# Kernel tuning notes

Measured on AMD Instinct MI355X. Metric: run time of the kernel, lower is better.

## Reference

```python
import jax, jax.numpy as jnp
import numpy as np

B, Q, D, H, P, F = 16, 300, 256, 8, 4, 2048
HG = WG = 100          # feature-map height/width (hw = 10000, perfect square)
HW = HG * WG
DH = D // H
EPS = 1e-5


def _ln(x, g, b):
    m = x.mean(-1, keepdims=True)
    v = jnp.var(x, axis=-1, keepdims=True)
    return (x - m) * jax.lax.rsqrt(v + EPS) * g + b


def setup_inputs() -> dict:
    key = jax.random.key(0)
    ks = jax.random.split(key, 24)
    rn = lambda k, shape, s=0.02: jax.random.normal(k, shape, jnp.float32) * s
    return {
        "tgt": jax.random.normal(ks[0], (B, Q, D), jnp.float32),
        "memory": jax.random.normal(ks[1], (B, HW, D), jnp.float32),
        "in_proj_w": rn(ks[2], (D, 3 * D)), "in_proj_b": rn(ks[3], (3 * D,)),
        "out_proj_w": rn(ks[4], (D, D)), "out_proj_b": rn(ks[5], (D,)),
        "norm1_g": jnp.ones((D,), jnp.float32), "norm1_b": jnp.zeros((D,), jnp.float32),
        "ref_w": rn(ks[6], (D, 2)), "ref_b": rn(ks[7], (2,)),
        "off_w": rn(ks[8], (D, H * P * 2)), "off_b": rn(ks[9], (H * P * 2,)),
        "attw_w": rn(ks[10], (D, H * P)), "attw_b": rn(ks[11], (H * P,)),
        "vproj_w": rn(ks[12], (D, D)), "vproj_b": rn(ks[13], (D,)),
        "oproj_w": rn(ks[14], (D, D)), "oproj_b": rn(ks[15], (D,)),
        "norm2_g": jnp.ones((D,), jnp.float32), "norm2_b": jnp.zeros((D,), jnp.float32),
        "lin1_w": rn(ks[16], (D, F)), "lin1_b": rn(ks[17], (F,)),
        "lin2_w": rn(ks[18], (F, D)), "lin2_b": rn(ks[19], (D,)),
        "norm3_g": jnp.ones((D,), jnp.float32), "norm3_b": jnp.zeros((D,), jnp.float32),
    }


def reference(tgt, memory, in_proj_w, in_proj_b, out_proj_w, out_proj_b,
              norm1_g, norm1_b, ref_w, ref_b, off_w, off_b, attw_w, attw_b,
              vproj_w, vproj_b, oproj_w, oproj_b, norm2_g, norm2_b,
              lin1_w, lin1_b, lin2_w, lin2_b, norm3_g, norm3_b):
    # ---- self-attention (nn.MultiheadAttention, eval mode: dropout = identity)
    qkv = tgt @ in_proj_w + in_proj_b                      # [B,Q,3D]
    q, k, v = jnp.split(qkv, 3, axis=-1)
    q = q.reshape(B, Q, H, DH)
    k = k.reshape(B, Q, H, DH)
    v = v.reshape(B, Q, H, DH)
    scores = jnp.einsum('bqhd,bkhd->bhqk', q, k) / jnp.sqrt(jnp.float32(DH))
    attn = jax.nn.softmax(scores, axis=-1)
    sa = jnp.einsum('bhqk,bkhd->bqhd', attn, v).reshape(B, Q, D) @ out_proj_w + out_proj_b
    x = _ln(tgt + sa, norm1_g, norm1_b)

    # ---- reference points
    ref = jax.nn.sigmoid(x @ ref_w + ref_b)                # [B,Q,2] in (0,1)

    # ---- deformable cross-attention
    offs = (x @ off_w + off_b).reshape(B, Q, H, P, 2)
    wts = jax.nn.softmax((x @ attw_w + attw_b).reshape(B, Q, H, P), axis=-1)
    vals = (memory @ vproj_w + vproj_b).reshape(B, HW, H, DH)
    loc = jnp.clip(ref[:, :, None, None, :] + offs, 0.0, 1.0)
    sx = loc[..., 0] * (WG - 1)
    sy = loc[..., 1] * (HG - 1)
    x0 = jnp.floor(sx)
    y0 = jnp.floor(sy)
    x0i = jnp.clip(x0.astype(jnp.int32), 0, WG - 1)
    y0i = jnp.clip(y0.astype(jnp.int32), 0, HG - 1)
    x1i = jnp.clip(x0i + 1, 0, WG - 1)
    y1i = jnp.clip(y0i + 1, 0, HG - 1)
    wx1 = sx - x0
    wx0 = 1.0 - wx1
    wy1 = sy - y0
    wy0 = 1.0 - wy1
    bi = jnp.arange(B)[:, None, None, None]
    hi = jnp.arange(H)[None, None, :, None]

    def gather(yi, xi):                                    # [B,Q,H,P,DH]
        return vals[bi, yi * WG + xi, hi]

    samp = (gather(y0i, x0i) * (wx0 * wy0)[..., None]
            + gather(y1i, x0i) * (wx0 * wy1)[..., None]
            + gather(y0i, x1i) * (wx1 * wy0)[..., None]
            + gather(y1i, x1i) * (wx1 * wy1)[..., None])
    ca = (samp * wts[..., None]).sum(axis=3).reshape(B, Q, D) @ oproj_w + oproj_b
    x = _ln(x + ca, norm2_g, norm2_b)

    # ---- FFN
    ff = jax.nn.relu(x @ lin1_w + lin1_b) @ lin2_w + lin2_b
    return _ln(x + ff, norm3_g, norm3_b)
```

## Files before the change

kernel.cpp:

```cpp
#include <hip/hip_runtime.h>

#define NB   16
#define NQ   300
#define ND   256
#define NH   8
#define NP   4
#define NF   2048
#define NHW  10000
#define NWG  100
#define NROW 4800

typedef __attribute__((ext_vector_type(8))) short bf16x8;
typedef __attribute__((ext_vector_type(4))) float f32x4;

__device__ __forceinline__ unsigned short f2bf(float f) {
    unsigned u = __builtin_bit_cast(unsigned, f);
    u = (u + 0x7fffu + ((u >> 16) & 1u)) >> 16;
    return (unsigned short)u;
}
__device__ __forceinline__ float bf2f(unsigned short h) {
    unsigned u = ((unsigned)h) << 16;
    return __builtin_bit_cast(float, u);
}

__device__ __forceinline__ bf16x8 cvt8(float4 lo, float4 hi) {
    unsigned r0, r1, r2, r3;
    asm("v_cvt_pk_bf16_f32 %0, %1, %2" : "=v"(r0) : "v"(lo.x), "v"(lo.y));
    asm("v_cvt_pk_bf16_f32 %0, %1, %2" : "=v"(r1) : "v"(lo.z), "v"(lo.w));
    asm("v_cvt_pk_bf16_f32 %0, %1, %2" : "=v"(r2) : "v"(hi.x), "v"(hi.y));
    asm("v_cvt_pk_bf16_f32 %0, %1, %2" : "=v"(r3) : "v"(hi.z), "v"(hi.w));
    uint4 u = {r0, r1, r2, r3};
    return __builtin_bit_cast(bf16x8, u);
}

__device__ __forceinline__ void gl_lds16(const unsigned short* g, unsigned short* l) {
    __builtin_amdgcn_global_load_lds(
        (__attribute__((address_space(1))) const void*)g,
        (__attribute__((address_space(3))) void*)l,
        16, 0, 0);
}
__device__ __forceinline__ void gl_lds16f(const float* g, float* l) {
    __builtin_amdgcn_global_load_lds(
        (__attribute__((address_space(1))) const void*)g,
        (__attribute__((address_space(3))) void*)l,
        16, 0, 0);
}

__global__ __launch_bounds__(256) void transpose_cast(
    const float* __restrict__ w_in,  const float* __restrict__ w_out,
    const float* __restrict__ w_vp,  const float* __restrict__ w_op,
    const float* __restrict__ w_l1,  const float* __restrict__ w_l2,
    unsigned short* __restrict__ o_in, unsigned short* __restrict__ o_out,
    unsigned short* __restrict__ o_vp, unsigned short* __restrict__ o_op,
    unsigned short* __restrict__ o_l1, unsigned short* __restrict__ o_l2)
{
    __shared__ float ts[64][65];
    int b = blockIdx.x;
    const float* src; unsigned short* dst; int K, N, ncx;
    if      (b < 48)  { src = w_in;  dst = o_in;  K = 256;  N = 768;  ncx = 12; }
    else if (b < 64)  { src = w_out; dst = o_out; K = 256;  N = 256;  ncx = 4;  b -= 48; }
    else if (b < 80)  { src = w_vp;  dst = o_vp;  K = 256;  N = 256;  ncx = 4;  b -= 64; }
    else if (b < 96)  { src = w_op;  dst = o_op;  K = 256;  N = 256;  ncx = 4;  b -= 80; }
    else if (b < 224) { src = w_l1;  dst = o_l1;  K = 256;  N = 2048; ncx = 32; b -= 96; }
    else              { src = w_l2;  dst = o_l2;  K = 2048; N = 256;  ncx = 4;  b -= 224; }
    const int n0 = (b % ncx) * 64, k0 = (b / ncx) * 64;
    const int t = threadIdx.x;
    const int r = t >> 4, c = t & 15;
    #pragma unroll
    for (int j = 0; j < 4; j++) {
        float4 v = *(const float4*)(src + (long)(k0 + j * 16 + r) * N + n0 + c * 4);
        ts[j * 16 + r][c * 4 + 0] = v.x;
        ts[j * 16 + r][c * 4 + 1] = v.y;
        ts[j * 16 + r][c * 4 + 2] = v.z;
        ts[j * 16 + r][c * 4 + 3] = v.w;
    }
    __syncthreads();
    #pragma unroll
    for (int j = 0; j < 4; j++) {
        unsigned short o[4];
        #pragma unroll
        for (int i = 0; i < 4; i++)
            o[i] = f2bf(ts[c * 4 + i][j * 16 + r]);
        *(uint2*)(dst + (long)(n0 + j * 16 + r) * K + k0 + c * 4) = *(uint2*)o;
    }
}

__global__ __launch_bounds__(256) void prep_head(
    const float* __restrict__ rw, const float* __restrict__ rb,
    const float* __restrict__ ow, const float* __restrict__ ob,
    const float* __restrict__ aw, const float* __restrict__ ab,
    unsigned short* __restrict__ o_hd, float* __restrict__ o_hb)
{
    int id = blockIdx.x * 256 + threadIdx.x;
    if (id < 32768) {
        int n = id >> 8, k = id & 255;
        float v;
        if (n < 2)       v = rw[k * 2 + n];
        else if (n < 66) v = ow[k * 64 + (n - 2)];
        else if (n < 98) v = aw[k * 32 + (n - 66)];
        else             v = 0.0f;
        o_hd[id] = f2bf(v);
        return;
    }
    id -= 32768;
    if (id < 128) {
        float v;
        if (id < 2)       v = rb[id];
        else if (id < 66) v = ob[id - 2];
        else if (id < 98) v = ab[id - 66];
        else              v = 0.0f;
        o_hb[id] = v;
    }
}

__global__ __launch_bounds__(512, 2) void gemm_vproj_bs(
    const float* __restrict__ A, const unsigned short* __restrict__ Bt,
    const float* __restrict__ bias, unsigned short* __restrict__ Cout)
{
    __shared__ __align__(16) unsigned short Bs[128 * 512];
    __shared__ __align__(16) float As[2][16 * 256];

    const int t    = threadIdx.x;
    const int wave = t >> 6, lane = t & 63;
    const int l16  = lane & 15, quad = lane >> 4;
    const long m0  = (long)blockIdx.x * 640;

    {
        const unsigned short* bp = Bt + (long)(wave * 32 + l16) * 256 + (quad << 3);
        unsigned short* bw = &Bs[wave << 13];
        #pragma unroll
        for (int kf = 0; kf < 8; kf++) {
            gl_lds16(bp + kf * 32,            bw + kf * 512);
            gl_lds16(bp + kf * 32 + 16 * 256, bw + 4096 + kf * 512);
        }
    }

    const float* aG = A + (m0 + l16) * 256 + wave * 32 + (quad << 3);
    auto issueA = [&](int it, int buf) {
        const float* g = aG + (long)it * 16 * 256;
        gl_lds16f(g,     &As[buf][wave * 512]);
        gl_lds16f(g + 4, &As[buf][wave * 512 + 256]);
    };

    issueA(0, 0);
    __syncthreads();

    float4 bj0 = *(const float4*)&bias[wave * 32 + (quad << 2)];
    float4 bj1 = *(const float4*)&bias[wave * 32 + 16 + (quad << 2)];

    const unsigned short* bF0 = &Bs[(wave << 13)] + (lane << 3);
    const unsigned short* bF1 = bF0 + 4096;

    for (int it = 0; it < 40; ++it) {
        const int cur = it & 1;
        if (it + 1 < 40) {
            issueA(it + 1, cur ^ 1);
            asm volatile("s_waitcnt vmcnt(2)" ::: "memory");
        } else {
            asm volatile("s_waitcnt vmcnt(0)" ::: "memory");
        }
        __builtin_amdgcn_sched_barrier(0);

        f32x4 acc0 = {0.f, 0.f, 0.f, 0.f}, acc1 = {0.f, 0.f, 0.f, 0.f};
        #pragma unroll
        for (int kf = 0; kf < 8; kf++) {
            const float4 alo = *(const float4*)&As[cur][kf * 512 + (lane << 2)];
            const float4 ahi = *(const float4*)&As[cur][kf * 512 + 256 + (lane << 2)];
            const bf16x8 af  = cvt8(alo, ahi);
            const bf16x8 bv0 = *(const bf16x8*)(bF0 + kf * 512);
            const bf16x8 bv1 = *(const bf16x8*)(bF1 + kf * 512);
            acc0 = __builtin_amdgcn_mfma_f32_16x16x32_bf16(bv0, af, acc0, 0, 0, 0);
            acc1 = __builtin_amdgcn_mfma_f32_16x16x32_bf16(bv1, af, acc1, 0, 0, 0);
        }

        const long gr = m0 + (long)it * 16 + l16;
        unsigned short* cp = Cout + gr * 256 + wave * 32 + (quad << 2);
        {
            unsigned short o[4] = {f2bf(acc0[0] + bj0.x), f2bf(acc0[1] + bj0.y),
                                   f2bf(acc0[2] + bj0.z), f2bf(acc0[3] + bj0.w)};
            *(uint2*)cp = *(uint2*)o;
        }
        {
            unsigned short o[4] = {f2bf(acc1[0] + bj1.x), f2bf(acc1[1] + bj1.y),
                                   f2bf(acc1[2] + bj1.z), f2bf(acc1[3] + bj1.w)};
            *(uint2*)(cp + 16) = *(uint2*)o;
        }

        __builtin_amdgcn_s_barrier();
    }
}

template <int RELU, int OUTBF, int SPLITK, int TM, int TN>
__global__ __launch_bounds__(TM * 4, 4) void gemm_bt(
    const float* __restrict__ A, const unsigned short* __restrict__ Bt,
    const float* __restrict__ bias, void* __restrict__ Cout,
    int M, int N, int K)
{
    constexpr int W   = TM / 16;
    constexpr int NFB = TN / 16;
    constexpr int WN  = TN / 64;
    constexpr int WM  = W / WN;
    constexpr int AI  = (TM / 16) / WM;
    constexpr int BPW = NFB / W;

    __shared__ __align__(16) unsigned short As[2][W * 512];
    __shared__ __align__(16) unsigned short Bs[2][NFB * 512];

    const int t    = threadIdx.x;
    const long m0  = (long)blockIdx.y * TM;
    const int  n0  = blockIdx.x * TN;
    const int  wave = t >> 6, lane = t & 63;
    const int  l16 = lane & 15, quad = lane >> 4;
    const int  wmi = wave / WN, wni = wave % WN;
    const int  wm  = wmi * (AI * 16);
    const int  wn  = wni * 64;
    const int  fA  = wmi * AI;
    const int  fB  = wni * 4;

    f32x4 acc[AI][4] = {};

    const int kChunk = K / SPLITK;
    const int kBeg   = (SPLITK > 1) ? blockIdx.z * kChunk : 0;
    const int nk     = kChunk / 32;

    const long aRow   = m0 + wave * 16 + l16;
    const bool aValid = (aRow < M);
    const float* aP   = A + aRow * (long)K + kBeg + (quad << 3);
    unsigned short* aW = &As[0][(wave << 9) + (lane << 3)];

    const unsigned short* bP =
        Bt + (long)(n0 + wave * (16 * BPW) + l16) * K + kBeg + (quad << 3);
    unsigned short* bW = &Bs[0][wave * BPW * 512];

    float4 la0 = make_float4(0.f, 0.f, 0.f, 0.f);
    float4 la1 = make_float4(0.f, 0.f, 0.f, 0.f);

    auto loadA = [&](int kt) {
        if (aValid) {
            la0 = *(const float4*)(aP + kt * 32);
            la1 = *(const float4*)(aP + kt * 32 + 4);
        }
    };
    auto writeA = [&](int buf) {
        const bf16x8 v = cvt8(la0, la1);
        *(bf16x8*)(aW + buf * (W * 512)) = v;
    };
    auto issueB = [&](int kt, int buf) {
        #pragma unroll
        for (int j = 0; j < BPW; j++)
            gl_lds16(bP + kt * 32 + (long)j * 16 * K,
                     bW + buf * (NFB * 512) + j * 512);
    };

    issueB(0, 0);
    loadA(0);
    writeA(0);
    __syncthreads();

    for (int kt = 0; kt < nk; kt++) {
        const int cur = kt & 1;
        if (kt + 1 < nk) {
            issueB(kt + 1, cur ^ 1);
            loadA(kt + 1);
        }

        bf16x8 af[AI], bfr[4];
        #pragma unroll
        for (int i = 0; i < AI; i++)
            af[i] = *(const bf16x8*)&As[cur][(fA + i) * 512 + (lane << 3)];
        #pragma unroll
        for (int j = 0; j < 4; j++)
            bfr[j] = *(const bf16x8*)&Bs[cur][(fB + j) * 512 + (lane << 3)];
        #pragma unroll
        for (int i = 0; i < AI; i++)
            #pragma unroll
            for (int j = 0; j < 4; j++)
                acc[i][j] = __builtin_amdgcn_mfma_f32_16x16x32_bf16(
                    bfr[j], af[i], acc[i][j], 0, 0, 0);

        if (kt + 1 < nk) {
            writeA(cur ^ 1);
            __syncthreads();
        }
    }

    float4 bj[4];
    #pragma unroll
    for (int j = 0; j < 4; j++)
        bj[j] = *(const float4*)&bias[n0 + wn + j * 16 + (quad << 2)];

    float* outp = (float*)Cout;
    float bscale = 1.0f;
    if (SPLITK > 1) {
        outp += (size_t)blockIdx.z * M * N;
        bscale = (blockIdx.z == 0) ? 1.0f : 0.0f;
    }

    #pragma unroll
    for (int i = 0; i < AI; i++) {
        const long gr = m0 + wm + i * 16 + l16;
        if (gr < M) {
            #pragma unroll
            for (int j = 0; j < 4; j++) {
                float4 v;
                v.x = acc[i][j][0] + bscale * bj[j].x;
                v.y = acc[i][j][1] + bscale * bj[j].y;
                v.z = acc[i][j][2] + bscale * bj[j].z;
                v.w = acc[i][j][3] + bscale * bj[j].w;
                if (RELU) {
                    v.x = fmaxf(v.x, 0.f); v.y = fmaxf(v.y, 0.f);
                    v.z = fmaxf(v.z, 0.f); v.w = fmaxf(v.w, 0.f);
                }
                const int gc = n0 + wn + j * 16 + (quad << 2);
                if (OUTBF) {
                    unsigned short o[4] = {f2bf(v.x), f2bf(v.y), f2bf(v.z), f2bf(v.w)};
                    *(uint2*)((unsigned short*)Cout + gr * N + gc) = *(uint2*)o;
                } else {
                    *(float4*)(outp + gr * N + gc) = v;
                }
            }
        }
    }
}

__global__ __launch_bounds__(256) void attn_kernel(
    const float* __restrict__ qkv, float* __restrict__ sa)
{
    __shared__ union {
        struct {
            unsigned short Ks[304][40];
            unsigned short Qs[64][40];
        } s;
        unsigned short Ps[4][16][328];
    } u;
    __shared__ unsigned short Vt[32][328];

    const int bh = blockIdx.y;
    const int b  = bh >> 3, h = bh & 7;
    const int q0 = blockIdx.x * 64;
    const int t  = threadIdx.x;

    for (int idx = t; idx < 304 * 8; idx += 256) {
        const int r = idx >> 3, c4 = (idx & 7) << 2;
        if (r < NQ) {
            const float4 kv = *(const float4*)(qkv + ((long)(b * NQ + r)) * 768 + 256 + h * 32 + c4);
            u.s.Ks[r][c4 + 0] = f2bf(kv.x); u.s.Ks[r][c4 + 1] = f2bf(kv.y);
            u.s.Ks[r][c4 + 2] = f2bf(kv.z); u.s.Ks[r][c4 + 3] = f2bf(kv.w);
        } else {
            u.s.Ks[r][c4 + 0] = 0; u.s.Ks[r][c4 + 1] = 0;
            u.s.Ks[r][c4 + 2] = 0; u.s.Ks[r][c4 + 3] = 0;
        }
    }
    for (int idx = t; idx < NQ * 8; idx += 256) {
        const int key = idx >> 3, dq = (idx & 7) << 2;
        const float4 vv = *(const float4*)(qkv + ((long)(b * NQ + key)) * 768 + 512 + h * 32 + dq);
        Vt[dq + 0][key] = f2bf(vv.x); Vt[dq + 1][key] = f2bf(vv.y);
        Vt[dq + 2][key] = f2bf(vv.z); Vt[dq + 3][key] = f2bf(vv.w);
    }
    for (int idx = t; idx < 32 * 20; idx += 256)
        Vt[idx / 20][300 + idx % 20] = 0;
    for (int idx = t; idx < 64 * 8; idx += 256) {
        const int r = idx >> 3, c4 = (idx & 7) << 2;
        const int q = q0 + r;
        if (q < NQ) {
            const float4 qv = *(const float4*)(qkv + ((long)(b * NQ + q)) * 768 + h * 32 + c4);
            u.s.Qs[r][c4 + 0] = f2bf(qv.x); u.s.Qs[r][c4 + 1] = f2bf(qv.y);
            u.s.Qs[r][c4 + 2] = f2bf(qv.z); u.s.Qs[r][c4 + 3] = f2bf(qv.w);
        } else {
            u.s.Qs[r][c4 + 0] = 0; u.s.Qs[r][c4 + 1] = 0;
            u.s.Qs[r][c4 + 2] = 0; u.s.Qs[r][c4 + 3] = 0;
        }
    }
    __syncthreads();

    const int wave = t >> 6, lane = t & 63;
    const int l16 = lane & 15, quad = lane >> 4;
    const float scale = 0.1767766952966369f;

    const bf16x8 aq = *(const bf16x8*)&u.s.Qs[wave * 16 + l16][quad * 8];
    f32x4 sacc[19];
    #pragma unroll
    for (int kt = 0; kt < 19; kt++) {
        const bf16x8 bk = *(const bf16x8*)&u.s.Ks[kt * 16 + l16][quad * 8];
        sacc[kt] = __builtin_amdgcn_mfma_f32_16x16x32_bf16(
            aq, bk, (f32x4){0.f, 0.f, 0.f, 0.f}, 0, 0, 0);
    }

    float inv[4];
    #pragma unroll
    for (int r = 0; r < 4; r++) {
        float m = -1e30f;
        #pragma unroll
        for (int kt = 0; kt < 19; kt++) {
            float s = sacc[kt][r] * scale;
            if (kt == 18 && l16 >= 12) s = -1e30f;
            sacc[kt][r] = s;
            m = fmaxf(m, s);
        }
        m = fmaxf(m, __shfl_xor(m, 1)); m = fmaxf(m, __shfl_xor(m, 2));
        m = fmaxf(m, __shfl_xor(m, 4)); m = fmaxf(m, __shfl_xor(m, 8));
        float sum = 0.f;
        #pragma unroll
        for (int kt = 0; kt < 19; kt++) {
            float p = __expf(sacc[kt][r] - m);
            sacc[kt][r] = p;
            sum += p;
        }
        sum += __shfl_xor(sum, 1); sum += __shfl_xor(sum, 2);
        sum += __shfl_xor(sum, 4); sum += __shfl_xor(sum, 8);
        inv[r] = 1.0f / sum;
    }

    __syncthreads();

    #pragma unroll
    for (int kt = 0; kt < 19; kt++)
        #pragma unroll
        for (int r = 0; r < 4; r++)
            u.Ps[wave][quad * 4 + r][kt * 16 + l16] = f2bf(sacc[kt][r] * inv[r]);
    #pragma unroll
    for (int r = 0; r < 4; r++)
        u.Ps[wave][quad * 4 + r][304 + l16] = 0;

    f32x4 o0 = {0.f, 0.f, 0.f, 0.f}, o1 = {0.f, 0.f, 0.f, 0.f};
    #pragma unroll
    for (int kt = 0; kt < 10; kt++) {
        const bf16x8 ap  = *(const bf16x8*)&u.Ps[wave][l16][kt * 32 + quad * 8];
        const bf16x8 bv0 = *(const bf16x8*)&Vt[l16][kt * 32 + quad * 8];
        const bf16x8 bv1 = *(const bf16x8*)&Vt[16 + l16][kt * 32 + quad * 8];
        o0 = __builtin_amdgcn_mfma_f32_16x16x32_bf16(ap, bv0, o0, 0, 0, 0);
        o1 = __builtin_amdgcn_mfma_f32_16x16x32_bf16(ap, bv1, o1, 0, 0, 0);
    }

    #pragma unroll
    for (int r = 0; r < 4; r++) {
        const int q = q0 + wave * 16 + quad * 4 + r;
        if (q < NQ) {
            float* op = sa + ((long)(b * NQ + q)) * ND + h * 32;
            op[l16]      = o0[r];
            op[16 + l16] = o1[r];
        }
    }
}

template <int NPART>
__global__ __launch_bounds__(256) void residual_ln(
    const float* __restrict__ a, const float* __restrict__ r,
    const float* __restrict__ gam, const float* __restrict__ bet,
    float* __restrict__ out, long pstride)
{
    const int row  = blockIdx.x * 4 + (threadIdx.x >> 6);
    const int lane = threadIdx.x & 63;
    const long base = (long)row * ND + lane * 4;
    float4 av = *(const float4*)(a + base);
    float4 rv = *(const float4*)(r + base);
    #pragma unroll
    for (int z = 1; z < NPART; z++) {
        float4 pv = *(const float4*)(r + z * pstride + base);
        rv.x += pv.x; rv.y += pv.y; rv.z += pv.z; rv.w += pv.w;
    }
    float x0 = av.x + rv.x, x1 = av.y + rv.y, x2 = av.z + rv.z, x3 = av.w + rv.w;
    float s  = x0 + x1 + x2 + x3;
    float s2 = x0 * x0 + x1 * x1 + x2 * x2 + x3 * x3;
    #pragma unroll
    for (int off = 32; off >= 1; off >>= 1) {
        s  += __shfl_xor(s, off);
        s2 += __shfl_xor(s2, off);
    }
    float mean = s * 0.00390625f;
    float var  = s2 * 0.00390625f - mean * mean;
    float rstd = rsqrtf(var + 1e-5f);
    float4 gv = *(const float4*)(gam + lane * 4);
    float4 bv = *(const float4*)(bet + lane * 4);
    float4 o;
    o.x = (x0 - mean) * rstd * gv.x + bv.x;
    o.y = (x1 - mean) * rstd * gv.y + bv.y;
    o.z = (x2 - mean) * rstd * gv.z + bv.z;
    o.w = (x3 - mean) * rstd * gv.w + bv.w;
    *(float4*)(out + base) = o;
}

__global__ __launch_bounds__(256) void meta_kernel(
    const float* __restrict__ res, float* __restrict__ meta)
{
    const int t   = threadIdx.x;
    const int row = blockIdx.x * 8 + (t >> 5);
    const int s   = t & 31;
    const int h   = s >> 2;
    const float* rp = res + (long)row * 128;
    const float rx = 1.f / (1.f + __expf(-rp[0]));
    const float ry = 1.f / (1.f + __expf(-rp[1]));
    const float offx = rp[2 + 2 * s], offy = rp[3 + 2 * s];
    const float a0 = rp[66 + h * 4 + 0], a1 = rp[66 + h * 4 + 1];
    const float a2 = rp[66 + h * 4 + 2], a3 = rp[66 + h * 4 + 3];
    const float mx = fmaxf(fmaxf(a0, a1), fmaxf(a2, a3));
    const float den = __expf(a0 - mx) + __expf(a1 - mx) +
                      __expf(a2 - mx) + __expf(a3 - mx);
    const float awt = __expf(rp[66 + s] - mx) / den;

    const float lx = fminf(fmaxf(rx + offx, 0.f), 1.f) * (NWG - 1);
    const float ly = fminf(fmaxf(ry + offy, 0.f), 1.f) * (NWG - 1);
    const float fx = floorf(lx), fy = floorf(ly);
    int x0 = (int)fx; x0 = min(max(x0, 0), NWG - 1);
    int y0 = (int)fy; y0 = min(max(y0, 0), NWG - 1);
    const int x1 = min(x0 + 1, NWG - 1);
    const int y1 = min(y0 + 1, NWG - 1);
    const float wx1 = lx - fx, wx0 = 1.f - wx1;
    const float wy1 = ly - fy, wy0 = 1.f - wy1;
    float4 m0, m1;
    m0.x = __int_as_float(y0 * NWG + x0);
    m0.y = __int_as_float(y0 * NWG + x1);
    m0.z = __int_as_float(y1 * NWG + x0);
    m0.w = __int_as_float(y1 * NWG + x1);
    m1.x = awt * wx0 * wy0;
    m1.y = awt * wx1 * wy0;
    m1.z = awt * wx0 * wy1;
    m1.w = awt * wx1 * wy1;
    float* mp = meta + (long)row * 256 + s * 8;
    *(float4*)mp       = m0;
    *(float4*)(mp + 4) = m1;
}

__global__ __launch_bounds__(256) void deform_gather(
    const float* __restrict__ meta, const unsigned short* __restrict__ vals,
    float* __restrict__ ca)
{
    const int row = blockIdx.x;
    const int b = row / NQ;
    __shared__ float ms[256];
    const int t = threadIdx.x;
    ms[t] = meta[(long)row * 256 + t];
    __syncthreads();
    const int h = t >> 5, d = t & 31;
    const unsigned short* vb = vals + (long)b * NHW * ND + h * 32 + d;
    float acc = 0.f;
    #pragma unroll
    for (int p = 0; p < NP; p++) {
        const float* mp = ms + h * 32 + p * 8;
        const int i00 = __float_as_int(mp[0]);
        const int i01 = __float_as_int(mp[1]);
        const int i10 = __float_as_int(mp[2]);
        const int i11 = __float_as_int(mp[3]);
        acc += mp[4] * bf2f(vb[(long)i00 * ND]);
        acc += mp[5] * bf2f(vb[(long)i01 * ND]);
        acc += mp[6] * bf2f(vb[(long)i10 * ND]);
        acc += mp[7] * bf2f(vb[(long)i11 * ND]);
    }
    ca[(long)row * ND + t] = acc;
}

extern "C" void kernel_launch(void* const* d_in, const int* in_sizes, int n_in,
                              void* d_out, int out_size, void* d_ws, size_t ws_size,
                              hipStream_t stream)
{
    (void)in_sizes; (void)n_in; (void)out_size; (void)ws_size;
    const float* tgt   = (const float*)d_in[0];
    const float* mem   = (const float*)d_in[1];
    const float* inpw  = (const float*)d_in[2];
    const float* inpb  = (const float*)d_in[3];
    const float* outw  = (const float*)d_in[4];
    const float* outb  = (const float*)d_in[5];
    const float* n1g   = (const float*)d_in[6];
    const float* n1b   = (const float*)d_in[7];
    const float* refw  = (const float*)d_in[8];
    const float* refb  = (const float*)d_in[9];
    const float* offw  = (const float*)d_in[10];
    const float* offb  = (const float*)d_in[11];
    const float* attww = (const float*)d_in[12];
    const float* attwb = (const float*)d_in[13];
    const float* vpw   = (const float*)d_in[14];
    const float* vpb   = (const float*)d_in[15];
    const float* opw   = (const float*)d_in[16];
    const float* opb   = (const float*)d_in[17];
    const float* n2g   = (const float*)d_in[18];
    const float* n2b   = (const float*)d_in[19];
    const float* l1w   = (const float*)d_in[20];
    const float* l1b   = (const float*)d_in[21];
    const float* l2w   = (const float*)d_in[22];
    const float* l2b   = (const float*)d_in[23];
    const float* n3g   = (const float*)d_in[24];
    const float* n3b   = (const float*)d_in[25];
    float* out = (float*)d_out;

    char* p = (char*)d_ws;
    auto alloc = [&](size_t bytes) {
        char* r = p; p += (bytes + 255) & ~(size_t)255; return (void*)r;
    };
    unsigned short* wtIn   = (unsigned short*)alloc(768 * 256 * 2);
    unsigned short* wtOut  = (unsigned short*)alloc(256 * 256 * 2);
    unsigned short* wtVp   = (unsigned short*)alloc(256 * 256 * 2);
    unsigned short* wtOp   = (unsigned short*)alloc(256 * 256 * 2);
    unsigned short* wtL1   = (unsigned short*)alloc(2048 * 256 * 2);
    unsigned short* wtL2   = (unsigned short*)alloc(256 * 2048 * 2);
    unsigned short* wtHead = (unsigned short*)alloc(128 * 256 * 2);
    float*          headb  = (float*)alloc(128 * 4);
    float* qkv  = (float*)alloc((size_t)NROW * 768 * 4);
    float* sa   = (float*)alloc((size_t)NROW * ND * 4);
    float* x1   = (float*)alloc((size_t)NROW * ND * 4);
    float* x2   = (float*)alloc((size_t)NROW * ND * 4);
    float* tmp  = (float*)alloc((size_t)NROW * ND * 4 * 4);
    float* ca   = (float*)alloc((size_t)NROW * ND * 4);
    float* meta = (float*)alloc((size_t)NROW * 256 * 4);
    void* uni = alloc((size_t)NB * NHW * ND * 2);
    unsigned short* vals = (unsigned short*)uni;
    float* h1 = (float*)uni;
    float* res = qkv;

    transpose_cast<<<352, 256, 0, stream>>>(
        inpw, outw, vpw, opw, l1w, l2w,
        wtIn, wtOut, wtVp, wtOp, wtL1, wtL2);
    prep_head<<<129, 256, 0, stream>>>(refw, refb, offw, offb, attww, attwb,
                                       wtHead, headb);

    gemm_bt<0, 0, 1, 64, 256><<<dim3(3, 75), 256, 0, stream>>>(tgt, wtIn, inpb, qkv,
                                                               NROW, 768, 256);
    gemm_vproj_bs<<<250, 512, 0, stream>>>(mem, wtVp, vpb, vals);
    attn_kernel<<<dim3(5, 128), 256, 0, stream>>>(qkv, sa);
    gemm_bt<0, 0, 2, 64, 256><<<dim3(1, 75, 2), 256, 0, stream>>>(sa, wtOut, outb, tmp,
                                                                  NROW, 256, 256);
    residual_ln<2><<<1200, 256, 0, stream>>>(tgt, tmp, n1g, n1b, x1,
                                             (long)NROW * 256);
    gemm_bt<0, 0, 1, 64, 128><<<dim3(1, 75), 256, 0, stream>>>(x1, wtHead, headb, res,
                                                               NROW, 128, 256);
    meta_kernel<<<600, 256, 0, stream>>>(res, meta);
    deform_gather<<<4800, 256, 0, stream>>>(meta, vals, ca);
    gemm_bt<0, 0, 2, 64, 256><<<dim3(1, 75, 2), 256, 0, stream>>>(ca, wtOp, opb, tmp,
                                                                  NROW, 256, 256);
    residual_ln<2><<<1200, 256, 0, stream>>>(x1, tmp, n2g, n2b, x2,
                                             (long)NROW * 256);
    gemm_bt<1, 0, 1, 64, 256><<<dim3(8, 75), 256, 0, stream>>>(x2, wtL1, l1b, h1,
                                                               NROW, 2048, 256);
    gemm_bt<0, 0, 4, 64, 256><<<dim3(1, 75, 4), 256, 0, stream>>>(h1, wtL2, l2b, tmp,
                                                                  NROW, 256, 2048);
    residual_ln<4><<<1200, 256, 0, stream>>>(x2, tmp, n3g, n3b, out,
                                             (long)NROW * 256);
}
```

Before: 470.1 us.

## Stream fp32 A tiles directly to LDS and convert at fragment load in gemm_bt

The generic GEMM now loads its fp32 A tile straight into LDS with direct global-to-LDS copies, alongside the bf16 B tile, instead of staging it through registers and writing bf16 to LDS. The fp32-to-bf16 conversion moves to fragment-load time, and synchronisation becomes explicit vmcnt waits plus raw barriers, which lets A and B prefetch overlap the MFMA work. The row-bounds check on M is removed, relying on M being a multiple of 64. A barrier is also added before compute in the fused vproj kernel. The cost is a larger fp32 A buffer in LDS and conversion work repeated by each wave that reads a fragment.

```diff
diff --git a/kernel.cpp b/kernel.cpp
--- a/kernel.cpp
+++ b/kernel.cpp
@@ -159,6 +159,7 @@
         } else {
             asm volatile("s_waitcnt vmcnt(0)" ::: "memory");
         }
+        __builtin_amdgcn_s_barrier();
         __builtin_amdgcn_sched_barrier(0);
 
         f32x4 acc0 = {0.f, 0.f, 0.f, 0.f}, acc1 = {0.f, 0.f, 0.f, 0.f};
@@ -190,24 +191,25 @@
     }
 }
 
-template <int RELU, int OUTBF, int SPLITK, int TM, int TN>
-__global__ __launch_bounds__(TM * 4, 4) void gemm_bt(
+template <int RELU, int OUTBF, int SPLITK, int TN>
+__global__ __launch_bounds__(256, 4) void gemm_bt(
     const float* __restrict__ A, const unsigned short* __restrict__ Bt,
     const float* __restrict__ bias, void* __restrict__ Cout,
     int M, int N, int K)
 {
-    constexpr int W   = TM / 16;
+    constexpr int W   = 4;
     constexpr int NFB = TN / 16;
     constexpr int WN  = TN / 64;
     constexpr int WM  = W / WN;
-    constexpr int AI  = (TM / 16) / WM;
+    constexpr int AI  = 4 / WM;
     constexpr int BPW = NFB / W;
-
-    __shared__ __align__(16) unsigned short As[2][W * 512];
+    constexpr int VC  = BPW + 2;
+
+    __shared__ __align__(16) float          Asf[2][4 * 512];
     __shared__ __align__(16) unsigned short Bs[2][NFB * 512];
 
     const int t    = threadIdx.x;
-    const long m0  = (long)blockIdx.y * TM;
+    const long m0  = (long)blockIdx.y * 64;
     const int  n0  = blockIdx.x * TN;
     const int  wave = t >> 6, lane = t & 63;
     const int  l16 = lane & 15, quad = lane >> 4;
@@ -223,51 +225,44 @@
     const int kBeg   = (SPLITK > 1) ? blockIdx.z * kChunk : 0;
     const int nk     = kChunk / 32;
 
-    const long aRow   = m0 + wave * 16 + l16;
-    const bool aValid = (aRow < M);
-    const float* aP   = A + aRow * (long)K + kBeg + (quad << 3);
-    unsigned short* aW = &As[0][(wave << 9) + (lane << 3)];
-
+    const float* aP = A + (m0 + wave * 16 + l16) * (long)K + kBeg + (quad << 3);
     const unsigned short* bP =
         Bt + (long)(n0 + wave * (16 * BPW) + l16) * K + kBeg + (quad << 3);
-    unsigned short* bW = &Bs[0][wave * BPW * 512];
-
-    float4 la0 = make_float4(0.f, 0.f, 0.f, 0.f);
-    float4 la1 = make_float4(0.f, 0.f, 0.f, 0.f);
-
-    auto loadA = [&](int kt) {
-        if (aValid) {
-            la0 = *(const float4*)(aP + kt * 32);
-            la1 = *(const float4*)(aP + kt * 32 + 4);
-        }
-    };
-    auto writeA = [&](int buf) {
-        const bf16x8 v = cvt8(la0, la1);
-        *(bf16x8*)(aW + buf * (W * 512)) = v;
-    };
-    auto issueB = [&](int kt, int buf) {
+
+    auto issueAB = [&](int kt, int buf) {
+        const float* ga = aP + kt * 32;
+        gl_lds16f(ga,     &Asf[buf][wave * 512]);
+        gl_lds16f(ga + 4, &Asf[buf][wave * 512 + 256]);
         #pragma unroll
         for (int j = 0; j < BPW; j++)
             gl_lds16(bP + kt * 32 + (long)j * 16 * K,
-                     bW + buf * (NFB * 512) + j * 512);
+                     &Bs[buf][(wave * BPW + j) * 512]);
     };
 
-    issueB(0, 0);
-    loadA(0);
-    writeA(0);
-    __syncthreads();
+    issueAB(0, 0);
 
     for (int kt = 0; kt < nk; kt++) {
         const int cur = kt & 1;
         if (kt + 1 < nk) {
-            issueB(kt + 1, cur ^ 1);
-            loadA(kt + 1);
-        }
+            issueAB(kt + 1, cur ^ 1);
+            if constexpr (VC == 6) {
+                asm volatile("s_waitcnt vmcnt(6)" ::: "memory");
+            } else {
+                asm volatile("s_waitcnt vmcnt(4)" ::: "memory");
+            }
+        } else {
+            asm volatile("s_waitcnt vmcnt(0)" ::: "memory");
+        }
+        __builtin_amdgcn_s_barrier();
+        __builtin_amdgcn_sched_barrier(0);
 
         bf16x8 af[AI], bfr[4];
         #pragma unroll
-        for (int i = 0; i < AI; i++)
-            af[i] = *(const bf16x8*)&As[cur][(fA + i) * 512 + (lane << 3)];
+        for (int i = 0; i < AI; i++) {
+            const float4 alo = *(const float4*)&Asf[cur][(fA + i) * 512 + (lane << 2)];
+            const float4 ahi = *(const float4*)&Asf[cur][(fA + i) * 512 + 256 + (lane << 2)];
+            af[i] = cvt8(alo, ahi);
+        }
         #pragma unroll
         for (int j = 0; j < 4; j++)
             bfr[j] = *(const bf16x8*)&Bs[cur][(fB + j) * 512 + (lane << 3)];
@@ -278,10 +273,7 @@
                 acc[i][j] = __builtin_amdgcn_mfma_f32_16x16x32_bf16(
                     bfr[j], af[i], acc[i][j], 0, 0, 0);
 
-        if (kt + 1 < nk) {
-            writeA(cur ^ 1);
-            __syncthreads();
-        }
+        __builtin_amdgcn_s_barrier();
     }
 
     float4 bj[4];
@@ -299,25 +291,23 @@
     #pragma unroll
     for (int i = 0; i < AI; i++) {
         const long gr = m0 + wm + i * 16 + l16;
-        if (gr < M) {
-            #pragma unroll
-            for (int j = 0; j < 4; j++) {
-                float4 v;
-                v.x = acc[i][j][0] + bscale * bj[j].x;
-                v.y = acc[i][j][1] + bscale * bj[j].y;
-                v.z = acc[i][j][2] + bscale * bj[j].z;
-                v.w = acc[i][j][3] + bscale * bj[j].w;
-                if (RELU) {
-                    v.x = fmaxf(v.x, 0.f); v.y = fmaxf(v.y, 0.f);
-                    v.z = fmaxf(v.z, 0.f); v.w = fmaxf(v.w, 0.f);
-                }
-                const int gc = n0 + wn + j * 16 + (quad << 2);
-                if (OUTBF) {
-                    unsigned short o[4] = {f2bf(v.x), f2bf(v.y), f2bf(v.z), f2bf(v.w)};
-                    *(uint2*)((unsigned short*)Cout + gr * N + gc) = *(uint2*)o;
-                } else {
-                    *(float4*)(outp + gr * N + gc) = v;
-                }
+        #pragma unroll
+        for (int j = 0; j < 4; j++) {
+            float4 v;
+            v.x = acc[i][j][0] + bscale * bj[j].x;
+            v.y = acc[i][j][1] + bscale * bj[j].y;
+            v.z = acc[i][j][2] + bscale * bj[j].z;
+            v.w = acc[i][j][3] + bscale * bj[j].w;
+            if (RELU) {
+                v.x = fmaxf(v.x, 0.f); v.y = fmaxf(v.y, 0.f);
+                v.z = fmaxf(v.z, 0.f); v.w = fmaxf(v.w, 0.f);
+            }
+            const int gc = n0 + wn + j * 16 + (quad << 2);
+            if (OUTBF) {
+                unsigned short o[4] = {f2bf(v.x), f2bf(v.y), f2bf(v.z), f2bf(v.w)};
+                *(uint2*)((unsigned short*)Cout + gr * N + gc) = *(uint2*)o;
+            } else {
+                *(float4*)(outp + gr * N + gc) = v;
             }
         }
     }
@@ -612,26 +602,26 @@
     prep_head<<<129, 256, 0, stream>>>(refw, refb, offw, offb, attww, attwb,
                                        wtHead, headb);
 
-    gemm_bt<0, 0, 1, 64, 256><<<dim3(3, 75), 256, 0, stream>>>(tgt, wtIn, inpb, qkv,
-                                                               NROW, 768, 256);
+    gemm_bt<0, 0, 1, 256><<<dim3(3, 75), 256, 0, stream>>>(tgt, wtIn, inpb, qkv,
+                                                           NROW, 768, 256);
     gemm_vproj_bs<<<250, 512, 0, stream>>>(mem, wtVp, vpb, vals);
     attn_kernel<<<dim3(5, 128), 256, 0, stream>>>(qkv, sa);
-    gemm_bt<0, 0, 2, 64, 256><<<dim3(1, 75, 2), 256, 0, stream>>>(sa, wtOut, outb, tmp,
-                                                                  NROW, 256, 256);
+    gemm_bt<0, 0, 2, 256><<<dim3(1, 75, 2), 256, 0, stream>>>(sa, wtOut, outb, tmp,
+                                                              NROW, 256, 256);
     residual_ln<2><<<1200, 256, 0, stream>>>(tgt, tmp, n1g, n1b, x1,
                                              (long)NROW * 256);
-    gemm_bt<0, 0, 1, 64, 128><<<dim3(1, 75), 256, 0, stream>>>(x1, wtHead, headb, res,
-                                                               NROW, 128, 256);
+    gemm_bt<0, 0, 1, 128><<<dim3(1, 75), 256, 0, stream>>>(x1, wtHead, headb, res,
+                                                           NROW, 128, 256);
     meta_kernel<<<600, 256, 0, stream>>>(res, meta);
     deform_gather<<<4800, 256, 0, stream>>>(meta, vals, ca);
-    gemm_bt<0, 0, 2, 64, 256><<<dim3(1, 75, 2), 256, 0, stream>>>(ca, wtOp, opb, tmp,
-                                                                  NROW, 256, 256);
+    gemm_bt<0, 0, 2, 256><<<dim3(1, 75, 2), 256, 0, stream>>>(ca, wtOp, opb, tmp,
+                                                              NROW, 256, 256);
     residual_ln<2><<<1200, 256, 0, stream>>>(x1, tmp, n2g, n2b, x2,
                                              (long)NROW * 256);
-    gemm_bt<1, 0, 1, 64, 256><<<dim3(8, 75), 256, 0, stream>>>(x2, wtL1, l1b, h1,
-                                                               NROW, 2048, 256);
-    gemm_bt<0, 0, 4, 64, 256><<<dim3(1, 75, 4), 256, 0, stream>>>(h1, wtL2, l2b, tmp,
-                                                                  NROW, 256, 2048);
+    gemm_bt<1, 0, 1, 256><<<dim3(8, 75), 256, 0, stream>>>(x2, wtL1, l1b, h1,
+                                                           NROW, 2048, 256);
+    gemm_bt<0, 0, 4, 256><<<dim3(1, 75, 4), 256, 0, stream>>>(h1, wtL2, l2b, tmp,
+                                                              NROW, 256, 2048);
     residual_ln<4><<<1200, 256, 0, stream>>>(x2, tmp, n3g, n3b, out,
                                              (long)NROW * 256);
 }
```

Result: no change. 475.7 us (+1.2%).
